# Kernel optimization log

Hardware: AMD Instinct MI355X
Metric: run time of the kernel (lower is better)

## Reference

```python
import jax, jax.numpy as jnp
import numpy as np

N, DIM, H = 4096, 768, 12
HD = DIM // H  # head_dim = 64


def setup_inputs() -> dict:
    key = jax.random.key(0)
    ks = jax.random.split(key, 7)
    std = 1.0 / np.sqrt(HD)
    return {
        "seq": jax.random.normal(ks[0], (N, DIM), dtype=jnp.float32),
        "Wq": jax.random.normal(ks[1], (H, HD, HD), dtype=jnp.float32) * std,
        "bq": jax.random.normal(ks[2], (H, HD), dtype=jnp.float32) * std,
        "Wk": jax.random.normal(ks[3], (H, HD, HD), dtype=jnp.float32) * std,
        "bk": jax.random.normal(ks[4], (H, HD), dtype=jnp.float32) * std,
        "Wv": jax.random.normal(ks[5], (H, HD, HD), dtype=jnp.float32) * std,
        "bv": jax.random.normal(ks[6], (H, HD), dtype=jnp.float32) * std,
    }


def reference(seq, Wq, bq, Wk, bk, Wv, bv):
    n = seq.shape[0]
    # split the feature dim into heads: [N, H, HD]
    s = seq.reshape(n, H, HD)
    # per-head linear projections (torch Linear: y = x W^T + b; W stored as [in,out])
    q = jnp.einsum("nhd,hde->hne", s, Wq) + bq[:, None, :]  # [H, N, HD]
    k = jnp.einsum("nhd,hde->hne", s, Wk) + bk[:, None, :]
    v = jnp.einsum("nhd,hde->hne", s, Wv) + bv[:, None, :]
    scale = 1.0 / jnp.sqrt(jnp.asarray(HD, dtype=seq.dtype))
    scores = jnp.einsum("hne,hme->hnm", q, k) * scale  # [H, N, N]
    attn = jax.nn.softmax(scores, axis=-1)
    out = jnp.einsum("hnm,hme->hne", attn, v)  # [H, N, HD]
    # hstack of per-head results == concat along features in head order
    return jnp.transpose(out, (1, 0, 2)).reshape(n, DIM)
```

## Files before the change

### kernel.cpp

```cpp
#include <hip/hip_runtime.h>
#include <stdint.h>
#include <stddef.h>

#define N   4096
#define DIM 768
#define H   12
#define HD  64

typedef __attribute__((ext_vector_type(4))) int   i32x4;
typedef __attribute__((ext_vector_type(4))) float f32x4;
typedef __attribute__((ext_vector_type(8))) short short8;

#define MFMA(acc, a, b) \
  acc = __builtin_amdgcn_mfma_f32_16x16x32_bf16(a, b, acc, 0, 0, 0)

#define GLOAD_LDS(gsrc, ldst) \
  __builtin_amdgcn_global_load_lds( \
      (const __attribute__((address_space(1))) uint32_t*)(gsrc), \
      (__attribute__((address_space(3))) uint32_t*)(ldst), 16, 0, 0)

static __device__ __forceinline__ float fast_exp2(float x) {
#if __has_builtin(__builtin_amdgcn_exp2f)
  return __builtin_amdgcn_exp2f(x);
#else
  return exp2f(x);
#endif
}

static __device__ __forceinline__ int pack_bf16(float lo, float hi) {
  const uint32_t ulo = __builtin_bit_cast(uint32_t, lo) + 0x8000u;
  const uint32_t uhi = __builtin_bit_cast(uint32_t, hi) + 0x8000u;
  return (int)__builtin_amdgcn_perm(uhi, ulo, 0x07060302u);
}

static __device__ __forceinline__ short to_bf16(float x) {
  union { float f; uint32_t u; } v; v.f = x;
  uint32_t u = v.u;
  u += 0x7fffu + ((u >> 16) & 1u);
  return (short)(u >> 16);
}

__global__ __launch_bounds__(256) void proj_kernel(
    const float* __restrict__ seq,
    const float* __restrict__ Wq, const float* __restrict__ bq,
    const float* __restrict__ Wk, const float* __restrict__ bk,
    const float* __restrict__ Wv, const float* __restrict__ bv,
    short* __restrict__ Qo, short* __restrict__ Ko, short* __restrict__ Vto)
{
  __shared__ float sT[64][36];
  const int h  = blockIdx.y;
  const int r0 = blockIdx.x * 32;
  const int t  = (int)threadIdx.x;

#pragma unroll
  for (int i = 0; i < 8; ++i) {
    const int idx = t + i * 256;
    const int r = idx >> 6, c = idx & 63;
    sT[c][r] = seq[(size_t)(r0 + r) * DIM + h * HD + c];
  }
  __syncthreads();

  const int w = t >> 6, l = t & 63;
  const int rb = w * 8;
  float aq[8], ak[8], av[8];
  const float bqv = bq[h * HD + l];
  const float bkv = bk[h * HD + l];
  const float bvv = bv[h * HD + l];
#pragma unroll
  for (int r = 0; r < 8; ++r) { aq[r] = bqv; ak[r] = bkv; av[r] = bvv; }

  const float* __restrict__ Wqb = Wq + h * 4096;
  const float* __restrict__ Wkb = Wk + h * 4096;
  const float* __restrict__ Wvb = Wv + h * 4096;

  float nq = Wqb[l], nk = Wkb[l], nv = Wvb[l];
#pragma unroll 8
  for (int d = 0; d < 64; ++d) {
    const float wq = nq, wk = nk, wv = nv;
    const int dn = ((d + 1) & 63) * 64 + l;
    nq = Wqb[dn]; nk = Wkb[dn]; nv = Wvb[dn];
    const f32x4* sp = (const f32x4*)&sT[d][rb];
    const f32x4 s0 = sp[0], s1 = sp[1];
#pragma unroll
    for (int r = 0; r < 4; ++r) {
      aq[r]     = fmaf(s0[r], wq, aq[r]);
      ak[r]     = fmaf(s0[r], wk, ak[r]);
      av[r]     = fmaf(s0[r], wv, av[r]);
      aq[4 + r] = fmaf(s1[r], wq, aq[4 + r]);
      ak[4 + r] = fmaf(s1[r], wk, ak[4 + r]);
      av[4 + r] = fmaf(s1[r], wv, av[4 + r]);
    }
  }

  const float QSC = 0.1803368801111204f;
#pragma unroll
  for (int r = 0; r < 8; ++r) {
    const int n = r0 + rb + r;
    Qo[((size_t)h * N + n) * HD + l] = to_bf16(aq[r] * QSC);
    Ko[((size_t)h * N + n) * HD + l] = to_bf16(ak[r]);
    const int loc = n & 63;
    const int ns  = (n & ~63) | ((loc & 0x1C) << 1) | ((loc & 32) >> 3) | (loc & 3);
    Vto[((size_t)h * HD + l) * N + ns] = to_bf16(av[r]);
  }
}

__global__ __launch_bounds__(256) void attn_kernel(
    const short* __restrict__ Q, const short* __restrict__ K,
    const short* __restrict__ Vt, float* __restrict__ out)
{
  __shared__ __align__(16) char lds[32768];

  const int h  = blockIdx.y;
  const int q0 = blockIdx.x * 64;
  const int t  = (int)threadIdx.x;
  const int w  = t >> 6, l = t & 63, lr = l & 15, lg = l >> 4;

  const short* __restrict__ Qw = Q + ((size_t)h * N + q0 + w * 16) * HD;
  const char*  __restrict__ Kb = (const char*)(K  + (size_t)h * N * HD);
  const char*  __restrict__ Vb = (const char*)(Vt + (size_t)h * HD * N);

  short8 qf[2];
#pragma unroll
  for (int ds = 0; ds < 2; ++ds)
    qf[ds] = *(const short8*)(Qw + lr * HD + ds * 32 + lg * 8);

  f32x4 o[4], o5;
  o5 = f32x4{0.f, 0.f, 0.f, 0.f};
#pragma unroll
  for (int eb = 0; eb < 4; ++eb) o[eb] = f32x4{0.f, 0.f, 0.f, 0.f};
  const short8 vones = {0x3F80, 0x3F80, 0x3F80, 0x3F80,
                        0x3F80, 0x3F80, 0x3F80, 0x3F80};

  const int c0   = w * 2;
  const int c1   = c0 + 1;
  const int sr0  = c0 * 8 + (l >> 3);
  const int sr1  = sr0 + 8;
  const int scol = ((l & 7) * 16) ^ ((l >> 3) << 4);
  const int kdo0 = c0 * 1024 + l * 16;
  const int kdo1 = c1 * 1024 + l * 16;
  const int ko0  = sr0 * 128 + scol;
  const int ko1  = sr1 * 128 + scol;
  const int vo0  = sr0 * (N * 2) + scol;
  const int vo1  = sr1 * (N * 2) + scol;

  GLOAD_LDS(Kb + ko0, lds + kdo0);
  GLOAD_LDS(Kb + ko1, lds + kdo1);
  GLOAD_LDS(Vb + vo0, lds + 8192 + kdo0);
  GLOAD_LDS(Vb + vo1, lds + 8192 + kdo1);
  __syncthreads();

  for (int it = 0; it < N / 64; ++it) {
    const int  j1 = (it + 1) * 64;
    const bool pf = j1 < N;
    if (pf) {
      char* const nb = lds + ((it + 1) & 1) * 16384;
      const char* kt = Kb + (size_t)j1 * 128;
      const char* vt = Vb + (size_t)j1 * 2;
      GLOAD_LDS(kt + ko0, nb + kdo0);
      GLOAD_LDS(kt + ko1, nb + kdo1);
      GLOAD_LDS(vt + vo0, nb + 8192 + kdo0);
      GLOAD_LDS(vt + vo1, nb + 8192 + kdo1);
    }
    const char* k_lds = lds + (it & 1) * 16384;
    const char* v_lds = k_lds + 8192;

    f32x4 s[4];
#pragma unroll
    for (int kb = 0; kb < 4; ++kb) {
      const int krow = kb * 16 + lr;
      const int kswz = (krow & 7) << 4;
      const char* kr = k_lds + krow * 128;
      const short8 kf0 = *(const short8*)(kr + ((lg * 16) ^ kswz));
      const short8 kf1 = *(const short8*)(kr + ((64 + lg * 16) ^ kswz));
      f32x4 acc = {0.f, 0.f, 0.f, 0.f};
      MFMA(acc, kf0, qf[0]);
      MFMA(acc, kf1, qf[1]);
      s[kb] = acc;
    }

#pragma unroll
    for (int kb = 0; kb < 4; ++kb)
#pragma unroll
      for (int r = 0; r < 4; ++r)
        s[kb][r] = fast_exp2(s[kb][r]);

    i32x4 p0, p1;
    p0[0] = pack_bf16(s[0][0], s[0][1]);
    p0[1] = pack_bf16(s[0][2], s[0][3]);
    p0[2] = pack_bf16(s[2][0], s[2][1]);
    p0[3] = pack_bf16(s[2][2], s[2][3]);
    p1[0] = pack_bf16(s[1][0], s[1][1]);
    p1[1] = pack_bf16(s[1][2], s[1][3]);
    p1[2] = pack_bf16(s[3][0], s[3][1]);
    p1[3] = pack_bf16(s[3][2], s[3][3]);
    const short8 pa0 = __builtin_bit_cast(short8, p0);
    const short8 pa1 = __builtin_bit_cast(short8, p1);

    MFMA(o5, pa0, vones);
    MFMA(o5, pa1, vones);
#pragma unroll
    for (int eb = 0; eb < 4; ++eb) {
      const int vrow = eb * 16 + lr;
      const int vswz = (vrow & 7) << 4;
      const char* vr = v_lds + vrow * 128;
      const short8 vf0 = *(const short8*)(vr + ((lg * 16) ^ vswz));
      const short8 vf1 = *(const short8*)(vr + ((64 + lg * 16) ^ vswz));
      MFMA(o[eb], pa0, vf0);
      MFMA(o[eb], pa1, vf1);
    }

    __syncthreads();
  }

#pragma unroll
  for (int r = 0; r < 4; ++r) {
    const float inv = 1.0f / o5[r];
    const int n = q0 + w * 16 + lg * 4 + r;
    float* orow = out + (size_t)n * DIM + h * HD;
#pragma unroll
    for (int eb = 0; eb < 4; ++eb)
      orow[eb * 16 + lr] = o[eb][r] * inv;
  }
}

extern "C" void kernel_launch(void* const* d_in, const int* in_sizes, int n_in,
                              void* d_out, int out_size, void* d_ws, size_t ws_size,
                              hipStream_t stream) {
  const float* seq = (const float*)d_in[0];
  const float* Wq  = (const float*)d_in[1];
  const float* bq  = (const float*)d_in[2];
  const float* Wk  = (const float*)d_in[3];
  const float* bk  = (const float*)d_in[4];
  const float* Wv  = (const float*)d_in[5];
  const float* bv  = (const float*)d_in[6];
  float* out = (float*)d_out;

  const size_t qkv = (size_t)H * N * HD;
  short* Qw  = (short*)d_ws;
  short* Kw  = Qw + qkv;
  short* Vtw = Kw + qkv;

  proj_kernel<<<dim3(N / 32, H), 256, 0, stream>>>(seq, Wq, bq, Wk, bk, Wv, bv,
                                                   Qw, Kw, Vtw);
  attn_kernel<<<dim3(N / 64, H), 256, 0, stream>>>(Qw, Kw, Vtw, out);
}
```

Measured before the change: 111.6 us.

## Compute QKV projection with split-bf16 MFMA instead of scalar FP32 FMAs

Adds a small kernel that transposes each weight matrix, folds in the Q scale, and splits it into bf16 high and low parts. The projection kernel then splits seq the same way and runs three-term bf16 MFMAs (hi*hi, lo*hi, hi*lo) to get close to FP32 accuracy on the matrix cores. This replaces the scalar FMA loop and the LDS transpose staging. In exchange it adds a third kernel launch and workspace for the split weights, and it slightly changes rounding.

```diff
diff --git a/kernel.cpp b/kernel.cpp
--- a/kernel.cpp
+++ b/kernel.cpp
@@ -40,67 +40,101 @@
   return (short)(u >> 16);
 }
 
+__global__ __launch_bounds__(256) void wsplit_kernel(
+    const float* __restrict__ Wq, const float* __restrict__ Wk,
+    const float* __restrict__ Wv, short* __restrict__ Whi,
+    short* __restrict__ Wlo)
+{
+  const int mh  = blockIdx.x;
+  const int mat = mh / 12;
+  const float* W = (mat == 0 ? Wq : (mat == 1 ? Wk : Wv)) + (mh % 12) * 4096;
+  const float scale = (mat == 0) ? 0.1803368801111204f : 1.0f;
+  __shared__ float T[64][65];
+  const int t = (int)threadIdx.x;
+#pragma unroll
+  for (int i = 0; i < 16; ++i) {
+    const int idx = t + i * 256;
+    T[idx & 63][idx >> 6] = W[idx] * scale;
+  }
+  __syncthreads();
+  short* hb = Whi + mh * 4096;
+  short* lb = Wlo + mh * 4096;
+#pragma unroll
+  for (int i = 0; i < 16; ++i) {
+    const int idx = t + i * 256;
+    const float wv = T[idx >> 6][idx & 63];
+    const uint32_t u = __builtin_bit_cast(uint32_t, wv);
+    const float hif = __builtin_bit_cast(float, u & 0xffff0000u);
+    hb[idx] = (short)(u >> 16);
+    lb[idx] = to_bf16(wv - hif);
+  }
+}
+
 __global__ __launch_bounds__(256) void proj_kernel(
     const float* __restrict__ seq,
-    const float* __restrict__ Wq, const float* __restrict__ bq,
-    const float* __restrict__ Wk, const float* __restrict__ bk,
-    const float* __restrict__ Wv, const float* __restrict__ bv,
+    const float* __restrict__ bq, const float* __restrict__ bk,
+    const float* __restrict__ bv,
+    const short* __restrict__ Whi, const short* __restrict__ Wlo,
     short* __restrict__ Qo, short* __restrict__ Ko, short* __restrict__ Vto)
 {
-  __shared__ float sT[64][36];
-  const int h  = blockIdx.y;
-  const int r0 = blockIdx.x * 32;
-  const int t  = (int)threadIdx.x;
-
-#pragma unroll
-  for (int i = 0; i < 8; ++i) {
-    const int idx = t + i * 256;
-    const int r = idx >> 6, c = idx & 63;
-    sT[c][r] = seq[(size_t)(r0 + r) * DIM + h * HD + c];
-  }
-  __syncthreads();
-
-  const int w = t >> 6, l = t & 63;
-  const int rb = w * 8;
-  float aq[8], ak[8], av[8];
-  const float bqv = bq[h * HD + l];
-  const float bkv = bk[h * HD + l];
-  const float bvv = bv[h * HD + l];
-#pragma unroll
-  for (int r = 0; r < 8; ++r) { aq[r] = bqv; ak[r] = bkv; av[r] = bvv; }
-
-  const float* __restrict__ Wqb = Wq + h * 4096;
-  const float* __restrict__ Wkb = Wk + h * 4096;
-  const float* __restrict__ Wvb = Wv + h * 4096;
-
-  float nq = Wqb[l], nk = Wkb[l], nv = Wvb[l];
-#pragma unroll 8
-  for (int d = 0; d < 64; ++d) {
-    const float wq = nq, wk = nk, wv = nv;
-    const int dn = ((d + 1) & 63) * 64 + l;
-    nq = Wqb[dn]; nk = Wkb[dn]; nv = Wvb[dn];
-    const f32x4* sp = (const f32x4*)&sT[d][rb];
-    const f32x4 s0 = sp[0], s1 = sp[1];
-#pragma unroll
-    for (int r = 0; r < 4; ++r) {
-      aq[r]     = fmaf(s0[r], wq, aq[r]);
-      ak[r]     = fmaf(s0[r], wk, ak[r]);
-      av[r]     = fmaf(s0[r], wv, av[r]);
-      aq[4 + r] = fmaf(s1[r], wq, aq[4 + r]);
-      ak[4 + r] = fmaf(s1[r], wk, ak[4 + r]);
-      av[4 + r] = fmaf(s1[r], wv, av[4 + r]);
-    }
-  }
+  const int h = blockIdx.y;
+  const int t = (int)threadIdx.x;
+  const int w = t >> 6, l = t & 63, lr = l & 15, lg = l >> 4;
+  const int r0 = blockIdx.x * 64 + w * 16;
+
+  const float* ar = seq + (size_t)(r0 + lr) * DIM + h * HD;
+  short8 ah[2], al[2];
+#pragma unroll
+  for (int hf = 0; hf < 2; ++hf)
+#pragma unroll
+    for (int j = 0; j < 8; ++j) {
+      const float x = ar[hf * 32 + lg * 8 + j];
+      const uint32_t u = __builtin_bit_cast(uint32_t, x);
+      ah[hf][j] = (short)(u >> 16);
+      const float hif = __builtin_bit_cast(float, u & 0xffff0000u);
+      al[hf][j] = to_bf16(x - hif);
+    }
+
+#define DO_MAT(WHP, WLP, DST)                                     \
+  do {                                                            \
+    _Pragma("unroll")                                             \
+    for (int et = 0; et < 4; ++et) {                              \
+      const short* wh = (WHP) + (et * 16 + lr) * 64 + lg * 8;     \
+      const short* wl = (WLP) + (et * 16 + lr) * 64 + lg * 8;     \
+      const short8 bh0 = *(const short8*)(wh);                    \
+      const short8 bh1 = *(const short8*)(wh + 32);               \
+      const short8 bl0 = *(const short8*)(wl);                    \
+      const short8 bl1 = *(const short8*)(wl + 32);               \
+      f32x4 acc = {0.f, 0.f, 0.f, 0.f};                           \
+      MFMA(acc, ah[0], bh0); MFMA(acc, ah[1], bh1);               \
+      MFMA(acc, al[0], bh0); MFMA(acc, al[1], bh1);               \
+      MFMA(acc, ah[0], bl0); MFMA(acc, ah[1], bl1);               \
+      DST[et] = acc;                                              \
+    }                                                             \
+  } while (0)
+
+  f32x4 dq[4], dk[4], dv[4];
+  DO_MAT(Whi + (0 * 12 + h) * 4096, Wlo + (0 * 12 + h) * 4096, dq);
+  DO_MAT(Whi + (1 * 12 + h) * 4096, Wlo + (1 * 12 + h) * 4096, dk);
+  DO_MAT(Whi + (2 * 12 + h) * 4096, Wlo + (2 * 12 + h) * 4096, dv);
+#undef DO_MAT
 
   const float QSC = 0.1803368801111204f;
 #pragma unroll
-  for (int r = 0; r < 8; ++r) {
-    const int n = r0 + rb + r;
-    Qo[((size_t)h * N + n) * HD + l] = to_bf16(aq[r] * QSC);
-    Ko[((size_t)h * N + n) * HD + l] = to_bf16(ak[r]);
-    const int loc = n & 63;
-    const int ns  = (n & ~63) | ((loc & 0x1C) << 1) | ((loc & 32) >> 3) | (loc & 3);
-    Vto[((size_t)h * HD + l) * N + ns] = to_bf16(av[r]);
+  for (int et = 0; et < 4; ++et) {
+    const int e = et * 16 + lr;
+    const float bqs = bq[h * HD + e] * QSC;
+    const float bks = bk[h * HD + e];
+    const float bvs = bv[h * HD + e];
+#pragma unroll
+    for (int rr = 0; rr < 4; ++rr) {
+      const int n = r0 + lg * 4 + rr;
+      Qo[((size_t)h * N + n) * HD + e] = to_bf16(dq[et][rr] + bqs);
+      Ko[((size_t)h * N + n) * HD + e] = to_bf16(dk[et][rr] + bks);
+      const int loc = n & 63;
+      const int ns  = (n & ~63) | ((loc & 0x1C) << 1) | ((loc & 32) >> 3) | (loc & 3);
+      Vto[((size_t)h * HD + e) * N + ns] = to_bf16(dv[et][rr] + bvs);
+    }
   }
 }
 
@@ -239,8 +273,11 @@
   short* Qw  = (short*)d_ws;
   short* Kw  = Qw + qkv;
   short* Vtw = Kw + qkv;
-
-  proj_kernel<<<dim3(N / 32, H), 256, 0, stream>>>(seq, Wq, bq, Wk, bk, Wv, bv,
+  short* Whi = Vtw + qkv;
+  short* Wlo = Whi + (size_t)3 * H * HD * HD;
+
+  wsplit_kernel<<<dim3(3 * H), 256, 0, stream>>>(Wq, Wk, Wv, Whi, Wlo);
+  proj_kernel<<<dim3(N / 64, H), 256, 0, stream>>>(seq, bq, bk, bv, Whi, Wlo,
                                                    Qw, Kw, Vtw);
   attn_kernel<<<dim3(N / 64, H), 256, 0, stream>>>(Qw, Kw, Vtw, out);
 }
```

After: 104.7 us. -6.2%, faster.
